# Optimization experiments

Measured on AMD Instinct MI355X. Metric: run time of the kernel, lower is better.

## Reference

```python
import jax, jax.numpy as jnp
import numpy as np

B, L, H = 2, 1024, 768
DI, N, K, R = 1536, 16, 4, 48


def setup_inputs() -> dict:
    key = jax.random.key(0)
    ks = jax.random.split(key, 10)
    s = 0.02
    inp = {
        "x": jax.random.normal(ks[0], (B, L, H), jnp.float32),
        "in_up_w": jax.random.normal(ks[1], (2 * DI * 4, H), jnp.float32) * s,
        "in_down_w": jax.random.normal(ks[2], (2 * DI, 2 * DI * 4), jnp.float32) * s,
        "conv_w": jax.random.normal(ks[3], (DI, 1, K), jnp.float32) * 0.5,
        "conv_b": jnp.zeros((DI,), jnp.float32),
        "x_proj_w": jax.random.normal(ks[4], (R + 2 * N, DI), jnp.float32) * s,
        "dt_w": jax.random.normal(ks[5], (DI, R), jnp.float32) * s,
        "dt_b": jnp.full((DI,), -4.0, jnp.float32) + jax.random.normal(ks[6], (DI,), jnp.float32) * 0.1,
        "A_log": jnp.log(jnp.broadcast_to(jnp.arange(1, N + 1, dtype=jnp.float32)[None, :], (DI, N))),
        "D": jnp.ones((DI,), jnp.float32),
        "out_up_w": jax.random.normal(ks[7], (4 * DI, DI), jnp.float32) * s,
        "out_down_w": jax.random.normal(ks[8], (H, 4 * DI), jnp.float32) * s,
    }
    return inp


def reference(x, in_up_w, in_down_w, conv_w, conv_b, x_proj_w, dt_w, dt_b,
              A_log, D, out_up_w, out_down_w):
    act = jax.nn.silu
    # in_up_proj -> act -> in_down_proj  (use_bias=False)
    proj = act(x @ in_up_w.T) @ in_down_w.T          # [B, L, 2*DI]
    proj = proj.transpose(0, 2, 1)                   # [B, 2*DI, L]
    hs, gate = jnp.split(proj, 2, axis=1)            # each [B, DI, L]

    # depthwise causal conv1d (pad left K-1, truncate to L) + SiLU
    k = conv_w.shape[-1]
    c = hs.shape[1]
    y = jax.lax.conv_general_dilated(
        hs, conv_w, window_strides=(1,), padding=[(k - 1, 0)],
        feature_group_count=c, dimension_numbers=("NCH", "OIH", "NCH"))
    hs = act(y + conv_b[None, :, None])              # [B, DI, L]

    # x_proj -> split into dt / B / C
    ssm_p = jnp.einsum("bdl,kd->blk", hs, x_proj_w)  # [B, L, R+2N]
    r = dt_w.shape[1]
    n = A_log.shape[1]
    ts, Bm, Cm = jnp.split(ssm_p, [r, r + n], axis=-1)
    dt = jax.nn.softplus(ts @ dt_w.T + dt_b)         # [B, L, DI]
    dt = dt.transpose(0, 2, 1)                       # [B, DI, L]

    A = -jnp.exp(A_log)                              # [DI, N]
    dA = jnp.exp(dt[..., None] * A[None, :, None, :])        # [B, DI, L, N]
    dBu = dt[..., None] * Bm[:, None, :, :] * hs[..., None]  # [B, DI, L, N]

    def step(s, inps):
        dA_t, dBu_t, C_t = inps          # [B,DI,N], [B,DI,N], [B,N]
        s = dA_t * s + dBu_t
        return s, jnp.einsum("bdn,bn->bd", s, C_t)

    s0 = jnp.zeros((x.shape[0], c, n), x.dtype)
    _, ys = jax.lax.scan(
        step, s0,
        (dA.transpose(2, 0, 1, 3), dBu.transpose(2, 0, 1, 3), Cm.transpose(1, 0, 2)))
    yscan = ys.transpose(1, 2, 0)                    # [B, DI, L]

    yscan = yscan + hs * D[None, :, None]
    yscan = yscan * act(gate)

    # out_up_proj -> act -> out_down_proj (use_bias=False)
    out = act(yscan.transpose(0, 2, 1) @ out_up_w.T) @ out_down_w.T  # [B, L, H]
    return out
```

## Files before the change

kernel.cpp:

```cpp
#include <hip/hip_runtime.h>
#include <hip/hip_bf16.h>
#include <cstdint>

#define B_   2
#define L_   1024
#define H_   768
#define DI_  1536
#define DI2_ 3072
#define DUP_ 12288
#define DOUT_ 6144
#define N_   16
#define R_   48
#define SPW  128
#define BL_  2048
#define C_   64
#define CL_  16

typedef __bf16 bf16x8 __attribute__((ext_vector_type(8)));
typedef float  f32x4  __attribute__((ext_vector_type(4)));
typedef unsigned int u32;

__device__ __forceinline__ float silu_f(float v) {
    return v / (1.f + __expf(-v));
}

__device__ __forceinline__ void async_ld16(const void* g, void* lds) {
    __builtin_amdgcn_global_load_lds(
        (const __attribute__((address_space(1))) u32*)g,
        (__attribute__((address_space(3))) u32*)lds, 16, 0, 0);
}

__global__ void cvt_bf16(const float* __restrict__ src, __bf16* __restrict__ dst, int n)
{
    const int i = (blockIdx.x * blockDim.x + threadIdx.x) * 8;
    if (i < n) {
        const float4 a = *(const float4*)(src + i);
        const float4 b = *(const float4*)(src + i + 4);
        bf16x8 v;
        v[0] = (__bf16)a.x; v[1] = (__bf16)a.y; v[2] = (__bf16)a.z; v[3] = (__bf16)a.w;
        v[4] = (__bf16)b.x; v[5] = (__bf16)b.y; v[6] = (__bf16)b.z; v[7] = (__bf16)b.w;
        *(bf16x8*)(dst + i) = v;
    }
}

__global__ void pad_xp(const float* __restrict__ xp, __bf16* __restrict__ dst)
{
    const int i = (blockIdx.x * blockDim.x + threadIdx.x) * 8;
    const int j = i / DI_;
    bf16x8 v;
    if (j < 80) {
        const float4 a = *(const float4*)(xp + i);
        const float4 b = *(const float4*)(xp + i + 4);
        v[0] = (__bf16)a.x; v[1] = (__bf16)a.y; v[2] = (__bf16)a.z; v[3] = (__bf16)a.w;
        v[4] = (__bf16)b.x; v[5] = (__bf16)b.y; v[6] = (__bf16)b.z; v[7] = (__bf16)b.w;
    } else {
        for (int k = 0; k < 8; ++k) v[k] = (__bf16)0.f;
    }
    *(bf16x8*)(dst + i) = v;
}

__global__ void transpose_dtw(const float* __restrict__ w, float* __restrict__ wT)
{
    const int i = blockIdx.x * blockDim.x + threadIdx.x;
    const int r = i / DI_, d = i % DI_;
    wT[i] = w[(size_t)d * R_ + r];
}

template<int EPI, int ATOMIC, typename OutT>
__global__ __launch_bounds__(256) void gemm_bf16(
    const __bf16* __restrict__ A, const __bf16* __restrict__ W, OutT* __restrict__ O,
    int M, int N, int Kslice, int lda, int ldw, int ldo)
{
    constexpr int BM = 128, BN = 128, BK = 32;
    __shared__ __bf16 As[BM * BK];
    __shared__ __bf16 Bs[BN * BK];

    const int tid  = threadIdx.x;
    const int bm   = blockIdx.x * BM;
    const int bn   = blockIdx.y * BN;
    const int kbase = blockIdx.z * Kslice;

    const int wave = tid >> 6, lane = tid & 63;
    const int wm = (wave >> 1) * 64, wn = (wave & 1) * 64;
    const int quad = lane >> 4, tr = lane & 15;

    const int srow = tid >> 2;
    const int skc  = ((tid & 3) ^ ((srow >> 1) & 3)) * 8;
    const __bf16* Ag0 = A + (size_t)(bm + srow) * lda + kbase + skc;
    const __bf16* Ag1 = A + (size_t)(bm + srow + 64) * lda + kbase + skc;
    const __bf16* Wg0 = W + (size_t)(bn + srow) * ldw + kbase + skc;
    const __bf16* Wg1 = W + (size_t)(bn + srow + 64) * ldw + kbase + skc;
    __bf16* Al0 = &As[tid * 8];
    __bf16* Al1 = &As[2048 + tid * 8];
    __bf16* Bl0 = &Bs[tid * 8];
    __bf16* Bl1 = &Bs[2048 + tid * 8];

    const int fsw = (quad ^ ((tr >> 1) & 3)) * 8;
    const __bf16* arp = &As[(wm + tr) * BK + fsw];
    const __bf16* brp = &Bs[(wn + tr) * BK + fsw];

    f32x4 acc[4][4];
#pragma unroll
    for (int i = 0; i < 4; ++i)
#pragma unroll
        for (int j = 0; j < 4; ++j) acc[i][j] = (f32x4){0.f, 0.f, 0.f, 0.f};

    for (int k0 = 0; k0 < Kslice; k0 += BK) {
        __syncthreads();
        async_ld16(Ag0 + k0, Al0);
        async_ld16(Ag1 + k0, Al1);
        async_ld16(Wg0 + k0, Bl0);
        async_ld16(Wg1 + k0, Bl1);
        __syncthreads();

        bf16x8 af[4], bfv[4];
#pragma unroll
        for (int i = 0; i < 4; ++i) af[i]  = *(const bf16x8*)(arp + i * 16 * BK);
#pragma unroll
        for (int j = 0; j < 4; ++j) bfv[j] = *(const bf16x8*)(brp + j * 16 * BK);
#pragma unroll
        for (int i = 0; i < 4; ++i)
#pragma unroll
            for (int j = 0; j < 4; ++j)
                acc[i][j] = __builtin_amdgcn_mfma_f32_16x16x32_bf16(af[i], bfv[j], acc[i][j], 0, 0, 0);
    }

#pragma unroll
    for (int i = 0; i < 4; ++i) {
        const int row = bm + wm + i * 16 + quad * 4;
#pragma unroll
        for (int j = 0; j < 4; ++j) {
            const int col = bn + wn + j * 16 + tr;
            OutT* op = O + (size_t)row * ldo + col;
#pragma unroll
            for (int r = 0; r < 4; ++r) {
                float v = acc[i][j][r];
                if (EPI == 1) v = silu_f(v);
                if (ATOMIC == 1) atomicAdd((float*)(op + (size_t)r * ldo), v);
                else             op[(size_t)r * ldo] = (OutT)v;
            }
        }
    }
}

template<int EPI, int ATOMIC, typename OutT>
__global__ __launch_bounds__(512, 2) void gemm256(
    const __bf16* __restrict__ A, const __bf16* __restrict__ W, OutT* __restrict__ O,
    int M, int N, int Kslice, int lda, int ldw, int ldo)
{
    extern __shared__ __bf16 S[];
    __bf16* AS = S;
    __bf16* BS = S + 32768;

    const int tid = threadIdx.x;

    const int nxy  = gridDim.x * gridDim.y;
    const int flat = blockIdx.x + gridDim.x * blockIdx.y;
    const int q    = nxy >> 3;
    const int swz  = (flat & 7) * q + (flat >> 3);
    const int bm   = (swz % gridDim.x) * 256;
    const int bn   = (swz / gridDim.x) * 256;
    const int kbase = blockIdx.z * Kslice;
    const int NT    = Kslice >> 5;

    const int srow = tid >> 2;
    const int skc  = ((tid & 3) ^ ((tid >> 3) & 3)) * 8;
    const __bf16* Ag = A + (size_t)(bm + srow) * lda + kbase + skc;
    const __bf16* Wg = W + (size_t)(bn + srow) * ldw + kbase + skc;
    const size_t ldA128 = (size_t)128 * lda;
    const size_t ldW128 = (size_t)128 * ldw;
    __bf16* Asl = AS + tid * 8;
    __bf16* Bsl = BS + tid * 8;

    auto stageA = [&](int t) {
        const int sl = (t & 3) * 8192;
        const __bf16* g = Ag + t * 32;
        async_ld16(g,          Asl + sl);
        async_ld16(g + ldA128, Asl + sl + 4096);
    };
    auto stageB = [&](int t) {
        const int sl = (t & 3) * 8192;
        const __bf16* g = Wg + t * 32;
        async_ld16(g,          Bsl + sl);
        async_ld16(g + ldW128, Bsl + sl + 4096);
    };

    const int wv = tid >> 6, lane = tid & 63;
    const int wr = wv >> 2, wc = wv & 3;
    const int quad = lane >> 4, tr = lane & 15;
    const int fsw = (quad ^ ((tr >> 1) & 3)) * 8;
    const __bf16* arp = AS + (wr * 128 + tr) * 32 + fsw;
    const __bf16* brp = BS + (wc * 64 + tr) * 32 + fsw;

    f32x4 acc[8][4];
#pragma unroll
    for (int i = 0; i < 8; ++i)
#pragma unroll
        for (int j = 0; j < 4; ++j) acc[i][j] = (f32x4){0.f, 0.f, 0.f, 0.f};

    const int npre = NT < 3 ? NT : 3;
    for (int t = 0; t < npre; ++t) { stageA(t); stageB(t); }
    __builtin_amdgcn_sched_barrier(0);
    if (NT > 3) asm volatile("s_waitcnt vmcnt(8)" ::: "memory");
    else        asm volatile("s_waitcnt vmcnt(0)" ::: "memory");
    __builtin_amdgcn_s_barrier();
    __builtin_amdgcn_sched_barrier(0);

    for (int g = 0; g < NT; ++g) {
        const int sl = (g & 3) * 8192;
        const __bf16* ar = arp + sl;
        const __bf16* br = brp + sl;
        bf16x8 a0[4], a1[4], bv[4];

#pragma unroll
        for (int f = 0; f < 4; ++f) a0[f] = *(const bf16x8*)(ar + f * 16 * 32);
#pragma unroll
        for (int j = 0; j < 4; ++j) bv[j] = *(const bf16x8*)(br + j * 16 * 32);
        if (g + 3 < NT) stageA(g + 3);
        __builtin_amdgcn_sched_barrier(0);
        __builtin_amdgcn_s_barrier();
        __builtin_amdgcn_sched_barrier(0);
        __builtin_amdgcn_s_setprio(1);
#pragma unroll
        for (int f = 0; f < 4; ++f)
#pragma unroll
            for (int j = 0; j < 4; ++j)
                acc[f][j] = __builtin_amdgcn_mfma_f32_16x16x32_bf16(a0[f], bv[j], acc[f][j], 0, 0, 0);
        __builtin_amdgcn_s_setprio(0);
        __builtin_amdgcn_sched_barrier(0);
        __builtin_amdgcn_s_barrier();
        __builtin_amdgcn_sched_barrier(0);

#pragma unroll
        for (int f = 0; f < 4; ++f) a1[f] = *(const bf16x8*)(ar + (64 + f * 16) * 32);
        if (g + 3 < NT) stageB(g + 3);
        __builtin_amdgcn_sched_barrier(0);
        __builtin_amdgcn_s_barrier();
        __builtin_amdgcn_sched_barrier(0);
        __builtin_amdgcn_s_setprio(1);
#pragma unroll
        for (int f = 0; f < 4; ++f)
#pragma unroll
            for (int j = 0; j < 4; ++j)
                acc[4 + f][j] = __builtin_amdgcn_mfma_f32_16x16x32_bf16(a1[f], bv[j], acc[4 + f][j], 0, 0, 0);
        __builtin_amdgcn_s_setprio(0);
        __builtin_amdgcn_sched_barrier(0);

        const int rem = NT - 1 - g;
        if (rem >= 3)      asm volatile("s_waitcnt vmcnt(8)" ::: "memory");
        else if (rem == 2) asm volatile("s_waitcnt vmcnt(4)" ::: "memory");
        else if (rem == 1) asm volatile("s_waitcnt vmcnt(0)" ::: "memory");
        if (rem > 0) {
            __builtin_amdgcn_s_barrier();
            __builtin_amdgcn_sched_barrier(0);
        }
    }

#pragma unroll
    for (int fi = 0; fi < 8; ++fi) {
        const int row = bm + wr * 128 + fi * 16 + quad * 4;
#pragma unroll
        for (int fj = 0; fj < 4; ++fj) {
            const int col = bn + wc * 64 + fj * 16 + tr;
            OutT* op = O + (size_t)row * ldo + col;
#pragma unroll
            for (int r = 0; r < 4; ++r) {
                float v = acc[fi][fj][r];
                if (EPI == 1) v = silu_f(v);
                if (ATOMIC == 1) atomicAdd((float*)(op + (size_t)r * ldo), v);
                else             op[(size_t)r * ldo] = (OutT)v;
            }
        }
    }
}

__global__ void conv_kernel(const float* __restrict__ P,
                            const float* __restrict__ cw, const float* __restrict__ cb,
                            float* __restrict__ HS, __bf16* __restrict__ HSb)
{
    const int t = blockIdx.x * blockDim.x + threadIdx.x;
    const int d = t % DI_;
    const int bl = t / DI_;
    const int l = bl % L_;
    const float4 w = *(const float4*)(cw + (size_t)d * 4);
    const float wk[4] = {w.x, w.y, w.z, w.w};
    float acc = cb[d];
#pragma unroll
    for (int k = 0; k < 4; ++k) {
        const int ls = l - 3 + k;
        if (ls >= 0)
            acc += wk[k] * P[(size_t)(bl - l + ls) * DI2_ + d];
    }
    const float h = silu_f(acc);
    HS[t]  = h;
    HSb[t] = (__bf16)h;
}

__global__ void dt_kernel(const float* __restrict__ SP, const float* __restrict__ dtwT,
                          const float* __restrict__ dtb, float* __restrict__ DT)
{
    const int t = blockIdx.x * blockDim.x + threadIdx.x;
    const int d = t % DI_;
    const int bl = t / DI_;
    const float* ts = SP + (size_t)bl * SPW;
    float s = dtb[d];
#pragma unroll
    for (int r4 = 0; r4 < R_ / 4; ++r4) {
        const float4 tv = *(const float4*)(ts + r4 * 4);
        const float* wp = dtwT + (size_t)r4 * 4 * DI_ + d;
        s += tv.x * wp[0] + tv.y * wp[DI_] + tv.z * wp[2 * DI_] + tv.w * wp[3 * DI_];
    }
    DT[t] = (s > 20.f) ? s : log1pf(__expf(s));
}

__global__ __launch_bounds__(256) void scan_pass1(
    const float* __restrict__ DT, const float* __restrict__ HS,
    const float* __restrict__ SP, const float* __restrict__ A_log,
    float* __restrict__ Aprod, float* __restrict__ Bacc)
{
    const int t = blockIdx.x * blockDim.x + threadIdx.x;
    const int d = t % DI_;
    const int y = t / DI_;
    const int c = y % C_;
    const int b = y / C_;
    float A[N_], s[N_], ap[N_];
    {
        const float4* alp = (const float4*)(A_log + (size_t)d * N_);
        const float4 a0 = alp[0], a1 = alp[1], a2 = alp[2], a3 = alp[3];
        const float av[N_] = {a0.x,a0.y,a0.z,a0.w, a1.x,a1.y,a1.z,a1.w,
                              a2.x,a2.y,a2.z,a2.w, a3.x,a3.y,a3.z,a3.w};
#pragma unroll
        for (int n = 0; n < N_; ++n) { A[n] = -__expf(av[n]); s[n] = 0.f; ap[n] = 1.f; }
    }
    for (int il = 0; il < CL_; ++il) {
        const size_t bl = (size_t)b * L_ + c * CL_ + il;
        const float dt = DT[bl * DI_ + d];
        const float hs = HS[bl * DI_ + d];
        const float4* Bp = (const float4*)(SP + bl * SPW + R_);
        const float4 b0 = Bp[0], b1 = Bp[1], b2 = Bp[2], b3 = Bp[3];
        const float Bv[N_] = {b0.x,b0.y,b0.z,b0.w, b1.x,b1.y,b1.z,b1.w,
                              b2.x,b2.y,b2.z,b2.w, b3.x,b3.y,b3.z,b3.w};
        const float dh = dt * hs;
#pragma unroll
        for (int n = 0; n < N_; ++n) {
            const float dA = __expf(dt * A[n]);
            s[n] = fmaf(dA, s[n], dh * Bv[n]);
            ap[n] *= dA;
        }
    }
    float4* Ap = (float4*)(Aprod + (size_t)t * N_);
    float4* Bc = (float4*)(Bacc  + (size_t)t * N_);
    Ap[0] = make_float4(ap[0], ap[1], ap[2], ap[3]);
    Ap[1] = make_float4(ap[4], ap[5], ap[6], ap[7]);
    Ap[2] = make_float4(ap[8], ap[9], ap[10], ap[11]);
    Ap[3] = make_float4(ap[12], ap[13], ap[14], ap[15]);
    Bc[0] = make_float4(s[0], s[1], s[2], s[3]);
    Bc[1] = make_float4(s[4], s[5], s[6], s[7]);
    Bc[2] = make_float4(s[8], s[9], s[10], s[11]);
    Bc[3] = make_float4(s[12], s[13], s[14], s[15]);
}

__global__ __launch_bounds__(256) void scan_pass2(
    const float* __restrict__ Aprod, const float* __restrict__ Bacc,
    float* __restrict__ Sinit)
{
    const int t = blockIdx.x * blockDim.x + threadIdx.x;
    const int n = t & (N_ - 1);
    const int d = (t >> 4) % DI_;
    const int b = (t >> 4) / DI_;
    float s = 0.f;
    for (int c = 0; c < C_; ++c) {
        const size_t idx = (((size_t)b * C_ + c) * DI_ + d) * N_ + n;
        Sinit[idx] = s;
        s = fmaf(Aprod[idx], s, Bacc[idx]);
    }
}

__global__ __launch_bounds__(256) void scan_pass3(
    const float* __restrict__ DT, const float* __restrict__ HS,
    const float* __restrict__ SP, const float* __restrict__ P,
    const float* __restrict__ A_log, const float* __restrict__ Dv,
    const float* __restrict__ Sinit, __bf16* __restrict__ Y)
{
    const int t = blockIdx.x * blockDim.x + threadIdx.x;
    const int d = t % DI_;
    const int y = t / DI_;
    const int c = y % C_;
    const int b = y / C_;
    float A[N_], s[N_];
    {
        const float4* alp = (const float4*)(A_log + (size_t)d * N_);
        const float4 a0 = alp[0], a1 = alp[1], a2 = alp[2], a3 = alp[3];
        const float av[N_] = {a0.x,a0.y,a0.z,a0.w, a1.x,a1.y,a1.z,a1.w,
                              a2.x,a2.y,a2.z,a2.w, a3.x,a3.y,a3.z,a3.w};
#pragma unroll
        for (int n = 0; n < N_; ++n) A[n] = -__expf(av[n]);
    }
    {
        const float4* sp = (const float4*)(Sinit + (size_t)t * N_);
        const float4 s0 = sp[0], s1 = sp[1], s2 = sp[2], s3 = sp[3];
        s[0]=s0.x; s[1]=s0.y; s[2]=s0.z; s[3]=s0.w;
        s[4]=s1.x; s[5]=s1.y; s[6]=s1.z; s[7]=s1.w;
        s[8]=s2.x; s[9]=s2.y; s[10]=s2.z; s[11]=s2.w;
        s[12]=s3.x; s[13]=s3.y; s[14]=s3.z; s[15]=s3.w;
    }
    const float Dd = Dv[d];
    for (int il = 0; il < CL_; ++il) {
        const size_t bl = (size_t)b * L_ + c * CL_ + il;
        const float dt = DT[bl * DI_ + d];
        const float hs = HS[bl * DI_ + d];
        const float4* Bp = (const float4*)(SP + bl * SPW + R_);
        const float4 b0 = Bp[0], b1 = Bp[1], b2 = Bp[2], b3 = Bp[3];
        const float4 c0 = Bp[4], c1 = Bp[5], c2 = Bp[6], c3 = Bp[7];
        const float Bv[N_] = {b0.x,b0.y,b0.z,b0.w, b1.x,b1.y,b1.z,b1.w,
                              b2.x,b2.y,b2.z,b2.w, b3.x,b3.y,b3.z,b3.w};
        const float Cv[N_] = {c0.x,c0.y,c0.z,c0.w, c1.x,c1.y,c1.z,c1.w,
                              c2.x,c2.y,c2.z,c2.w, c3.x,c3.y,c3.z,c3.w};
        const float dh = dt * hs;
        float acc = 0.f;
#pragma unroll
        for (int n = 0; n < N_; ++n) {
            const float dA = __expf(dt * A[n]);
            s[n] = fmaf(dA, s[n], dh * Bv[n]);
            acc = fmaf(s[n], Cv[n], acc);
        }
        const float g = P[bl * DI2_ + DI_ + d];
        Y[bl * DI_ + d] = (__bf16)((acc + hs * Dd) * silu_f(g));
    }
}

extern "C" void kernel_launch(void* const* d_in, const int* in_sizes, int n_in,
                              void* d_out, int out_size, void* d_ws, size_t ws_size,
                              hipStream_t stream) {
    const float* x        = (const float*)d_in[0];
    const float* w_up     = (const float*)d_in[1];
    const float* w_down   = (const float*)d_in[2];
    const float* conv_w   = (const float*)d_in[3];
    const float* conv_b   = (const float*)d_in[4];
    const float* x_proj_w = (const float*)d_in[5];
    const float* dt_w     = (const float*)d_in[6];
    const float* dt_b     = (const float*)d_in[7];
    const float* A_log    = (const float*)d_in[8];
    const float* Dvec     = (const float*)d_in[9];
    const float* w_oup    = (const float*)d_in[10];
    const float* w_odown  = (const float*)d_in[11];
    float* out = (float*)d_out;

    static bool attr_done = []() {
        hipFuncSetAttribute(reinterpret_cast<const void*>(&gemm256<0, 1, float>),
                            hipFuncAttributeMaxDynamicSharedMemorySize, 131072);
        hipFuncSetAttribute(reinterpret_cast<const void*>(&gemm256<1, 0, __bf16>),
                            hipFuncAttributeMaxDynamicSharedMemorySize, 131072);
        return true;
    }();
    (void)attr_done;

    char* base = (char*)d_ws;
    __bf16* x_b      = (__bf16*)base;
    __bf16* wup_b    = (__bf16*)(base + 3145728);
    float*  P        = (float*)base;
    char* r2 = base + 25165824;
    __bf16* wdown_b  = (__bf16*)r2;
    __bf16* HSb      = (__bf16*)r2;
    float*  SPb      = (float*)(r2 + 6291456);
    float*  DTb      = (float*)(r2 + 7340032);
    __bf16* Yb       = (__bf16*)(r2 + 19922944);
    __bf16* XPpad    = (__bf16*)(r2 + 26214400);
    float*  dtwT     = (float*)(r2 + 26607616);
    __bf16* woup_b   = (__bf16*)(r2 + 26902528);
    __bf16* wodown_b = (__bf16*)(r2 + 45776896);
    char* r3 = r2 + 75497472;
    __bf16* U1b      = (__bf16*)r3;
    __bf16* U2b      = (__bf16*)r3;
    float*  Aprod    = (float*)r3;
    float*  Bacc     = (float*)(r3 + 12582912);
    float*  Sinit    = (float*)(r3 + 25165824);
    char* r4 = r3 + 50331648;
    float*  HS       = (float*)r4;

    cvt_bf16<<<(BL_ * H_) / 2048, 256, 0, stream>>>(x, x_b, BL_ * H_);
    cvt_bf16<<<(DUP_ * H_) / 2048, 256, 0, stream>>>(w_up, wup_b, DUP_ * H_);
    cvt_bf16<<<(DI2_ * DUP_) / 2048, 256, 0, stream>>>(w_down, wdown_b, DI2_ * DUP_);

    gemm_bf16<1, 0, __bf16><<<dim3(16, 96, 1), 256, 0, stream>>>(
        x_b, wup_b, U1b, BL_, DUP_, H_, H_, H_, DUP_);

    hipMemsetAsync(P, 0, (size_t)BL_ * DI2_ * 4, stream);
    gemm256<0, 1, float><<<dim3(8, 12, 8), 512, 131072, stream>>>(
        U1b, wdown_b, P, BL_, DI2_, DUP_ / 8, DUP_, DUP_, DI2_);

    pad_xp<<<(128 * DI_) / 2048, 256, 0, stream>>>(x_proj_w, XPpad);
    transpose_dtw<<<(R_ * DI_) / 256, 256, 0, stream>>>(dt_w, dtwT);
    cvt_bf16<<<(DOUT_ * DI_) / 2048, 256, 0, stream>>>(w_oup, woup_b, DOUT_ * DI_);
    cvt_bf16<<<(H_ * DOUT_) / 2048, 256, 0, stream>>>(w_odown, wodown_b, H_ * DOUT_);

    conv_kernel<<<(BL_ * DI_) / 256, 256, 0, stream>>>(P, conv_w, conv_b, HS, HSb);

    hipMemsetAsync(SPb, 0, (size_t)BL_ * SPW * 4, stream);
    gemm_bf16<0, 1, float><<<dim3(16, 1, 4), 256, 0, stream>>>(
        HSb, XPpad, SPb, BL_, SPW, DI_ / 4, DI_, DI_, SPW);

    dt_kernel<<<(BL_ * DI_) / 256, 256, 0, stream>>>(SPb, dtwT, dt_b, DTb);

    scan_pass1<<<(B_ * C_ * DI_) / 256, 256, 0, stream>>>(DTb, HS, SPb, A_log, Aprod, Bacc);
    scan_pass2<<<(B_ * DI_ * N_) / 256, 256, 0, stream>>>(Aprod, Bacc, Sinit);
    scan_pass3<<<(B_ * C_ * DI_) / 256, 256, 0, stream>>>(
        DTb, HS, SPb, P, A_log, Dvec, Sinit, Yb);

    gemm256<1, 0, __bf16><<<dim3(8, 24, 1), 512, 131072, stream>>>(
        Yb, woup_b, U2b, BL_, DOUT_, DI_, DI_, DI_, DOUT_);

    hipMemsetAsync(out, 0, (size_t)BL_ * H_ * 4, stream);
    gemm_bf16<0, 1, float><<<dim3(16, 6, 8), 256, 0, stream>>>(
        U2b, wodown_b, out, BL_, H_, DOUT_ / 8, DOUT_, DOUT_, H_);
}
```

Before: 889.5 us.

## Restructure gemm256 main loop into double-buffered 64-wide K tiles with quarter staging

```diff
diff --git a/kernel.cpp b/kernel.cpp
--- a/kernel.cpp
+++ b/kernel.cpp
@@ -143,6 +143,21 @@
     }
 }
 
+#define GATE_BAR(Nimm)                                          \
+    asm volatile("s_waitcnt vmcnt(" #Nimm ")" ::: "memory");    \
+    __builtin_amdgcn_sched_barrier(0);                          \
+    __builtin_amdgcn_s_barrier();                               \
+    __builtin_amdgcn_sched_barrier(0);
+
+#define MFMA16(J0, J1, AF, B0, B1)                              \
+    __builtin_amdgcn_s_setprio(1);                              \
+    _Pragma("unroll")                                           \
+    for (int f = 0; f < 8; ++f) {                               \
+        acc[f][J0] = __builtin_amdgcn_mfma_f32_16x16x32_bf16(AF[f], B0, acc[f][J0], 0, 0, 0); \
+        acc[f][J1] = __builtin_amdgcn_mfma_f32_16x16x32_bf16(AF[f], B1, acc[f][J1], 0, 0, 0); \
+    }                                                           \
+    __builtin_amdgcn_s_setprio(0);
+
 template<int EPI, int ATOMIC, typename OutT>
 __global__ __launch_bounds__(512, 2) void gemm256(
     const __bf16* __restrict__ A, const __bf16* __restrict__ W, OutT* __restrict__ O,
@@ -161,7 +176,7 @@
     const int bm   = (swz % gridDim.x) * 256;
     const int bn   = (swz / gridDim.x) * 256;
     const int kbase = blockIdx.z * Kslice;
-    const int NT    = Kslice >> 5;
+    const int NT    = Kslice >> 6;
 
     const int srow = tid >> 2;
     const int skc  = ((tid & 3) ^ ((tid >> 3) & 3)) * 8;
@@ -172,25 +187,25 @@
     __bf16* Asl = AS + tid * 8;
     __bf16* Bsl = BS + tid * 8;
 
-    auto stageA = [&](int t) {
-        const int sl = (t & 3) * 8192;
-        const __bf16* g = Ag + t * 32;
-        async_ld16(g,          Asl + sl);
-        async_ld16(g + ldA128, Asl + sl + 4096);
-    };
-    auto stageB = [&](int t) {
-        const int sl = (t & 3) * 8192;
-        const __bf16* g = Wg + t * 32;
-        async_ld16(g,          Bsl + sl);
-        async_ld16(g + ldW128, Bsl + sl + 4096);
+    auto stage = [&](int t, int pc) {
+        const int off = (t & 1) * 16384 + (pc >> 1) * 8192;
+        if (pc & 1) {
+            const __bf16* g = Wg + t * 64 + (pc >> 1) * 32;
+            async_ld16(g,          Bsl + off);
+            async_ld16(g + ldW128, Bsl + off + 4096);
+        } else {
+            const __bf16* g = Ag + t * 64 + (pc >> 1) * 32;
+            async_ld16(g,          Asl + off);
+            async_ld16(g + ldA128, Asl + off + 4096);
+        }
     };
 
     const int wv = tid >> 6, lane = tid & 63;
     const int wr = wv >> 2, wc = wv & 3;
     const int quad = lane >> 4, tr = lane & 15;
     const int fsw = (quad ^ ((tr >> 1) & 3)) * 8;
-    const __bf16* arp = AS + (wr * 128 + tr) * 32 + fsw;
-    const __bf16* brp = BS + (wc * 64 + tr) * 32 + fsw;
+    const __bf16* arp = AS + wr * 4096 + tr * 32 + fsw;
+    const __bf16* brp = BS + (wc >> 1) * 4096 + ((wc & 1) * 64 + tr) * 32 + fsw;
 
     f32x4 acc[8][4];
 #pragma unroll
@@ -198,62 +213,59 @@
 #pragma unroll
         for (int j = 0; j < 4; ++j) acc[i][j] = (f32x4){0.f, 0.f, 0.f, 0.f};
 
-    const int npre = NT < 3 ? NT : 3;
-    for (int t = 0; t < npre; ++t) { stageA(t); stageB(t); }
-    __builtin_amdgcn_sched_barrier(0);
-    if (NT > 3) asm volatile("s_waitcnt vmcnt(8)" ::: "memory");
-    else        asm volatile("s_waitcnt vmcnt(0)" ::: "memory");
-    __builtin_amdgcn_s_barrier();
-    __builtin_amdgcn_sched_barrier(0);
-
-    for (int g = 0; g < NT; ++g) {
-        const int sl = (g & 3) * 8192;
+    stage(0, 0); stage(0, 1); stage(0, 2); stage(0, 3);
+    GATE_BAR(4)
+
+    for (int t = 0; t < NT - 1; ++t) {
+        const int sl = (t & 1) * 16384;
         const __bf16* ar = arp + sl;
         const __bf16* br = brp + sl;
-        bf16x8 a0[4], a1[4], bv[4];
-
-#pragma unroll
-        for (int f = 0; f < 4; ++f) a0[f] = *(const bf16x8*)(ar + f * 16 * 32);
-#pragma unroll
-        for (int j = 0; j < 4; ++j) bv[j] = *(const bf16x8*)(br + j * 16 * 32);
-        if (g + 3 < NT) stageA(g + 3);
-        __builtin_amdgcn_sched_barrier(0);
-        __builtin_amdgcn_s_barrier();
-        __builtin_amdgcn_sched_barrier(0);
-        __builtin_amdgcn_s_setprio(1);
-#pragma unroll
-        for (int f = 0; f < 4; ++f)
-#pragma unroll
-            for (int j = 0; j < 4; ++j)
-                acc[f][j] = __builtin_amdgcn_mfma_f32_16x16x32_bf16(a0[f], bv[j], acc[f][j], 0, 0, 0);
-        __builtin_amdgcn_s_setprio(0);
-        __builtin_amdgcn_sched_barrier(0);
-        __builtin_amdgcn_s_barrier();
-        __builtin_amdgcn_sched_barrier(0);
-
-#pragma unroll
-        for (int f = 0; f < 4; ++f) a1[f] = *(const bf16x8*)(ar + (64 + f * 16) * 32);
-        if (g + 3 < NT) stageB(g + 3);
-        __builtin_amdgcn_sched_barrier(0);
-        __builtin_amdgcn_s_barrier();
-        __builtin_amdgcn_sched_barrier(0);
-        __builtin_amdgcn_s_setprio(1);
-#pragma unroll
-        for (int f = 0; f < 4; ++f)
-#pragma unroll
-            for (int j = 0; j < 4; ++j)
-                acc[4 + f][j] = __builtin_amdgcn_mfma_f32_16x16x32_bf16(a1[f], bv[j], acc[4 + f][j], 0, 0, 0);
-        __builtin_amdgcn_s_setprio(0);
-        __builtin_amdgcn_sched_barrier(0);
-
-        const int rem = NT - 1 - g;
-        if (rem >= 3)      asm volatile("s_waitcnt vmcnt(8)" ::: "memory");
-        else if (rem == 2) asm volatile("s_waitcnt vmcnt(4)" ::: "memory");
-        else if (rem == 1) asm volatile("s_waitcnt vmcnt(0)" ::: "memory");
-        if (rem > 0) {
-            __builtin_amdgcn_s_barrier();
-            __builtin_amdgcn_sched_barrier(0);
-        }
+        bf16x8 af[8], b0, b1;
+#pragma unroll
+        for (int f = 0; f < 8; ++f) af[f] = *(const bf16x8*)(ar + f * 512);
+        b0 = *(const bf16x8*)(br);
+        b1 = *(const bf16x8*)(br + 512);
+        stage(t + 1, 0);
+        MFMA16(0, 1, af, b0, b1)
+        b0 = *(const bf16x8*)(br + 1024);
+        b1 = *(const bf16x8*)(br + 1536);
+        stage(t + 1, 1);
+        MFMA16(2, 3, af, b0, b1)
+        GATE_BAR(4)
+#pragma unroll
+        for (int f = 0; f < 8; ++f) af[f] = *(const bf16x8*)(ar + 8192 + f * 512);
+        b0 = *(const bf16x8*)(br + 8192);
+        b1 = *(const bf16x8*)(br + 8192 + 512);
+        stage(t + 1, 2);
+        MFMA16(0, 1, af, b0, b1)
+        b0 = *(const bf16x8*)(br + 8192 + 1024);
+        b1 = *(const bf16x8*)(br + 8192 + 1536);
+        stage(t + 1, 3);
+        MFMA16(2, 3, af, b0, b1)
+        GATE_BAR(4)
+    }
+    {
+        const int sl = ((NT - 1) & 1) * 16384;
+        const __bf16* ar = arp + sl;
+        const __bf16* br = brp + sl;
+        bf16x8 af[8], b0, b1;
+#pragma unroll
+        for (int f = 0; f < 8; ++f) af[f] = *(const bf16x8*)(ar + f * 512);
+        b0 = *(const bf16x8*)(br);
+        b1 = *(const bf16x8*)(br + 512);
+        MFMA16(0, 1, af, b0, b1)
+        b0 = *(const bf16x8*)(br + 1024);
+        b1 = *(const bf16x8*)(br + 1536);
+        MFMA16(2, 3, af, b0, b1)
+        GATE_BAR(0)
+#pragma unroll
+        for (int f = 0; f < 8; ++f) af[f] = *(const bf16x8*)(ar + 8192 + f * 512);
+        b0 = *(const bf16x8*)(br + 8192);
+        b1 = *(const bf16x8*)(br + 8192 + 512);
+        MFMA16(0, 1, af, b0, b1)
+        b0 = *(const bf16x8*)(br + 8192 + 1024);
+        b1 = *(const bf16x8*)(br + 8192 + 1536);
+        MFMA16(2, 3, af, b0, b1)
     }
 
 #pragma unroll
```

Result: faster. 871.7 us (-2.0%).
